# Kernel optimization log

Measured on AMD Instinct MI355X. Metric: run time of the kernel, lower is better.

The kernel has to match this reference:

```python
import jax, jax.numpy as jnp
import numpy as np

N = 50000   # nodes
E = 800000  # edges
B = 64      # graphs in batch
IN = 128    # in_features
HID = 64    # hidden_channels
H = 4       # head_count
C = 10      # out_classes
NEG = 0.2   # leaky relu negative slope
EPS = 1e-5  # batchnorm eps (eval mode, running mean 0 / var 1)


def _gat(x, edge_index, W, a_src, a_dst, b):
    """PyG GATConv (add_self_loops=False, concat=True), eval mode (no dropout)."""
    Hh, F = a_src.shape
    xW = (x @ W).reshape(-1, Hh, F)                       # [N,H,F]
    src, dst = edge_index[0], edge_index[1]
    e = (jnp.einsum('nhf,hf->nh', xW, a_src)[src]
         + jnp.einsum('nhf,hf->nh', xW, a_dst)[dst])      # [E,H]
    e = jnp.where(e > 0, e, NEG * e)                      # leaky relu
    m = jax.ops.segment_max(e, dst, num_segments=N)       # per-dst max
    m = jnp.where(jnp.isfinite(m), m, 0.0)
    p = jnp.exp(e - m[dst])
    denom = jax.ops.segment_sum(p, dst, num_segments=N)
    alpha = p / jnp.maximum(denom[dst], 1e-16)            # edge softmax over dst
    out = jax.ops.segment_sum(alpha[:, :, None] * xW[src], dst, num_segments=N)
    return out.reshape(-1, Hh * F) + b


def _bn_relu(y, g, be):
    # BatchNorm1d in eval mode with running_mean=0, running_var=1, then ReLU
    return jax.nn.relu(g * y / jnp.sqrt(1.0 + EPS) + be)


def setup_inputs():
    key = jax.random.key(0)
    ks = jax.random.split(key, 24)
    s = lambda k, shape: (jax.random.normal(k, shape, jnp.float32) * 0.05)
    z = lambda shape: jnp.zeros(shape, jnp.float32)
    o = lambda shape: jnp.ones(shape, jnp.float32)
    return {
        'acc_flag': 0,
        'x': jax.random.normal(ks[0], (N, IN), jnp.float32),
        'edge_index': jax.random.randint(ks[1], (2, E), 0, N),
        'batch': jnp.sort(jax.random.randint(ks[2], (N,), 0, B)),
        # layer 1: GATConv(IN -> HID, heads=H, concat)
        'W1': s(ks[3], (IN, H * HID)), 'a_src1': s(ks[4], (H, HID)), 'a_dst1': s(ks[5], (H, HID)), 'b1': z((H * HID,)),
        # proj: GATConv(H*HID -> HID, heads=1) + BN
        'W2': s(ks[6], (H * HID, HID)), 'a_src2': s(ks[7], (1, HID)), 'a_dst2': s(ks[8], (1, HID)), 'b2': z((HID,)), 'g2': o((HID,)), 'be2': z((HID,)),
        # block 1
        'W3': s(ks[9], (HID, HID)), 'a_src3': s(ks[10], (1, HID)), 'a_dst3': s(ks[11], (1, HID)), 'b3': z((HID,)), 'g3': o((HID,)), 'be3': z((HID,)),
        # block 2
        'W4': s(ks[12], (HID, HID)), 'a_src4': s(ks[13], (1, HID)), 'a_dst4': s(ks[14], (1, HID)), 'b4': z((HID,)), 'g4': o((HID,)), 'be4': z((HID,)),
        # MLP head
        'Wh1': s(ks[15], (HID, 128)), 'bh1': z((128,)),
        'Wh2': s(ks[16], (128, C)), 'bh2': z((C,)),
    }


def reference(acc_flag, x, edge_index, batch,
              W1, a_src1, a_dst1, b1,
              W2, a_src2, a_dst2, b2, g2, be2,
              W3, a_src3, a_dst3, b3, g3, be3,
              W4, a_src4, a_dst4, b4, g4, be4,
              Wh1, bh1, Wh2, bh2):
    # hardware GAT layer + ReLU (relu applied twice in original -> idempotent)
    x1 = jax.nn.relu(_gat(x, edge_index, W1, a_src1, a_dst1, b1))   # [N, H*HID]
    # projection block: residual base is zeros (shape mismatch H*HID vs HID)
    h = _bn_relu(_gat(x1, edge_index, W2, a_src2, a_dst2, b2), g2, be2)
    # residual blocks (shapes match -> x + relu(bn(y)))
    h = h + _bn_relu(_gat(h, edge_index, W3, a_src3, a_dst3, b3), g3, be3)
    h = h + _bn_relu(_gat(h, edge_index, W4, a_src4, a_dst4, b4), g4, be4)
    # global mean pool over graphs
    pooled = jax.ops.segment_sum(h, batch, num_segments=B)
    cnt = jnp.maximum(jax.ops.segment_sum(jnp.ones((N,), h.dtype), batch, num_segments=B), 1.0)
    hp = pooled / cnt[:, None]                                      # [B, HID]
    # MLP head
    return jax.nn.relu(hp @ Wh1 + bh1) @ Wh2 + bh2                  # [B, C]
```

## Files before the change

### kernel.cpp

```cpp
#include <hip/hip_runtime.h>

#define N_NODES 50000
#define N_EDGES 800000
#define N_GRAPHS 64
#define NEG_SLOPE 0.2f
#define BN_RSQ 0.9999950000374997f
#define NB_SCAN ((N_NODES + 255) / 256)

typedef __bf16 bf16x8 __attribute__((ext_vector_type(8)));
typedef float floatx4 __attribute__((ext_vector_type(4)));

__device__ __forceinline__ float lrelu(float v) { return v > 0.0f ? v : NEG_SLOPE * v; }

__device__ __forceinline__ float b2f(unsigned short u) {
    return __uint_as_float(((unsigned int)u) << 16);
}
__device__ __forceinline__ unsigned short f2b(float f) {
    unsigned int u = __float_as_uint(f);
    return (unsigned short)((u + 0x7fffu + ((u >> 16) & 1u)) >> 16);
}
__device__ __forceinline__ float blo(unsigned int d) { return __uint_as_float(d << 16); }
__device__ __forceinline__ float bhi(unsigned int d) { return __uint_as_float(d & 0xffff0000u); }

__global__ void k_deg(const int* __restrict__ ei, int* __restrict__ deg) {
    int e = blockIdx.x * blockDim.x + threadIdx.x;
    if (e < N_EDGES) atomicAdd(&deg[ei[N_EDGES + e]], 1);
}

__global__ __launch_bounds__(256) void k_offs(const int* __restrict__ deg, int* __restrict__ offs,
                                              int* __restrict__ total, const int* __restrict__ batch,
                                              int* __restrict__ bounds, int* __restrict__ bh) {
    __shared__ int lh[64];
    if (threadIdx.x < 64) lh[threadIdx.x] = 0;
    __syncthreads();
    if (blockIdx.x == 0 && threadIdx.x <= N_GRAPHS) {
        int g = threadIdx.x;
        int lo = 0, hi = N_NODES;
        while (lo < hi) {
            int mid = (lo + hi) >> 1;
            if (batch[mid] < g) lo = mid + 1; else hi = mid;
        }
        bounds[g] = lo;
    }
    int i = blockIdx.x * blockDim.x + threadIdx.x;
    int lane = threadIdx.x & 63;
    int v = (i < N_NODES) ? deg[i] : 0;
    int incl = v;
    for (int o = 1; o < 64; o <<= 1) {
        int t = __shfl_up(incl, o);
        if (lane >= o) incl += t;
    }
    int wtot = __shfl(incl, 63);
    int base = 0;
    if (lane == 0) base = atomicAdd(total, wtot);
    base = __shfl(base, 0);
    if (i < N_NODES) {
        offs[i] = base + incl - v;
        atomicAdd(&lh[min(v, 63)], 1);
    }
    __syncthreads();
    if (threadIdx.x < 64) bh[blockIdx.x * 64 + threadIdx.x] = lh[threadIdx.x];
}

__global__ __launch_bounds__(256) void k_pscan(const int* __restrict__ bh, int* __restrict__ bb) {
    __shared__ int partial[4][64];
    __shared__ int bbase[64];
    const int tid = threadIdx.x;
    const int b = tid & 63, q = tid >> 6;
    const int per = (NB_SCAN + 3) / 4;
    const int k0 = q * per, k1 = min(k0 + per, NB_SCAN);
    int s = 0;
    for (int k = k0; k < k1; ++k) s += bh[k * 64 + b];
    partial[q][b] = s;
    __syncthreads();
    if (tid < 64) {
        int tot = partial[0][tid] + partial[1][tid] + partial[2][tid] + partial[3][tid];
        int incl = tot;
        for (int o = 1; o < 64; o <<= 1) {
            int t2 = __shfl_up(incl, o);
            if (tid >= o) incl += t2;
        }
        bbase[tid] = incl - tot;
    }
    __syncthreads();
    int run = bbase[b];
    for (int q2 = 0; q2 < q; ++q2) run += partial[q2][b];
    for (int k = k0; k < k1; ++k) {
        bb[k * 64 + b] = run;
        run += bh[k * 64 + b];
    }
}

__global__ __launch_bounds__(256) void k_perm(const int* __restrict__ deg,
                                              const int* __restrict__ bb,
                                              int* __restrict__ perm) {
    __shared__ int lcnt[64];
    if (threadIdx.x < 64) lcnt[threadIdx.x] = 0;
    __syncthreads();
    int i = blockIdx.x * 256 + threadIdx.x;
    if (i < N_NODES) {
        int b = min(deg[i], 63);
        int r = atomicAdd(&lcnt[b], 1);
        perm[bb[blockIdx.x * 64 + b] + r] = i;
    }
}

__global__ void k_fill(const int* __restrict__ ei, const int* __restrict__ offs,
                       int* __restrict__ cur, int* __restrict__ csr_src) {
    int e = blockIdx.x * blockDim.x + threadIdx.x;
    if (e < N_EDGES) {
        int d = ei[N_EDGES + e];
        int pos = offs[d] + atomicAdd(&cur[d], 1);
        csr_src[pos] = ei[e];
    }
}

__global__ void k_prepw(const float* __restrict__ W1, const float* __restrict__ W2,
                        const float* __restrict__ W3, const float* __restrict__ W4,
                        unsigned short* __restrict__ Wt1, unsigned short* __restrict__ Wt2,
                        unsigned short* __restrict__ Wt3, unsigned short* __restrict__ Wt4) {
    int i = blockIdx.x * blockDim.x + threadIdx.x;
    if (i < 32768) {
        int k = i >> 8, n = i & 255;
        Wt1[n * 128 + k] = f2b(W1[i]);
    } else if (i < 49152) {
        int j = i - 32768;
        int k = j >> 6, n = j & 63;
        Wt2[n * 256 + k] = f2b(W2[j]);
    } else if (i < 53248) {
        int j = i - 49152;
        int k = j >> 6, n = j & 63;
        Wt3[n * 64 + k] = f2b(W3[j]);
    } else if (i < 57344) {
        int j = i - 53248;
        int k = j >> 6, n = j & 63;
        Wt4[n * 64 + k] = f2b(W4[j]);
    }
}

template <int K, int N, int HEADS, bool AF32>
__global__ __launch_bounds__(256) void k_mgemm(const void* __restrict__ Ap,
                                               const unsigned short* __restrict__ Bt,
                                               const float* __restrict__ asrc,
                                               const float* __restrict__ adst,
                                               unsigned short* __restrict__ out,
                                               float* __restrict__ es,
                                               float* __restrict__ ed, int rows) {
    constexpr int LDP = K + 8;
    __shared__ unsigned short As[64 * LDP];
    const int tid = threadIdx.x;
    const int r0 = blockIdx.x * 64;
    if (AF32) {
        const float* A = (const float*)Ap;
        for (int i = tid; i < 16 * K; i += 256) {
            int r = i / (K / 4), c4 = i % (K / 4);
            int row = r0 + r;
            float4 v = (row < rows) ? *(const float4*)&A[(size_t)row * K + c4 * 4]
                                    : make_float4(0.f, 0.f, 0.f, 0.f);
            ushort4 u;
            u.x = f2b(v.x); u.y = f2b(v.y); u.z = f2b(v.z); u.w = f2b(v.w);
            *(ushort4*)&As[r * LDP + c4 * 4] = u;
        }
    } else {
        const unsigned short* A = (const unsigned short*)Ap;
        for (int i = tid; i < 8 * K; i += 256) {
            int r = i / (K / 8), c8 = i % (K / 8);
            int row = r0 + r;
            uint4 v;
            if (row < rows) v = *(const uint4*)&A[(size_t)row * K + c8 * 8];
            else { v.x = v.y = v.z = v.w = 0; }
            *(uint4*)&As[r * LDP + c8 * 8] = v;
        }
    }
    __syncthreads();
    const int w = tid >> 6, lane = tid & 63;
    const int quad = lane >> 4, l16 = lane & 15;
    const int gr0 = r0 + w * 16 + quad * 4;
    bf16x8 afrag[K / 32];
#pragma unroll
    for (int kk = 0; kk < K / 32; ++kk)
        afrag[kk] = *(const bf16x8*)&As[(w * 16 + l16) * LDP + kk * 32 + quad * 8];
    float sacc[4] = {0.f, 0.f, 0.f, 0.f};
    float dacc[4] = {0.f, 0.f, 0.f, 0.f};
#pragma unroll 1
    for (int ct = 0; ct < N / 16; ++ct) {
        floatx4 acc = {0.f, 0.f, 0.f, 0.f};
#pragma unroll
        for (int kk = 0; kk < K / 32; ++kk) {
            const bf16x8 bfrag =
                *(const bf16x8*)&Bt[(size_t)(ct * 16 + l16) * K + kk * 32 + quad * 8];
            acc = __builtin_amdgcn_mfma_f32_16x16x32_bf16(afrag[kk], bfrag, acc, 0, 0, 0);
        }
        const int gc = ct * 16 + l16;
        const int hh = gc >> 6;
        const int f = gc & 63;
        const float as = asrc[hh * 64 + f];
        const float ad = adst[hh * 64 + f];
#pragma unroll
        for (int rg = 0; rg < 4; ++rg) {
            sacc[rg] = fmaf(acc[rg], as, sacc[rg]);
            dacc[rg] = fmaf(acc[rg], ad, dacc[rg]);
        }
#pragma unroll
        for (int rg = 0; rg < 4; ++rg) {
            int gr = gr0 + rg;
            if (gr < rows) out[(size_t)gr * N + gc] = f2b(acc[rg]);
        }
        if ((ct & 3) == 3) {
#pragma unroll
            for (int rg = 0; rg < 4; ++rg) {
                float s = sacc[rg], d = dacc[rg];
                for (int o = 1; o < 16; o <<= 1) {
                    s += __shfl_xor(s, o);
                    d += __shfl_xor(d, o);
                }
                if (l16 == 0) {
                    int gr = gr0 + rg;
                    if (gr < rows) {
                        es[(size_t)gr * HEADS + hh] = s;
                        ed[(size_t)gr * HEADS + hh] = d;
                    }
                }
                sacc[rg] = 0.f;
                dacc[rg] = 0.f;
            }
        }
    }
}

__global__ __launch_bounds__(256) void k_gat1(
    const unsigned short* __restrict__ xW, const float* __restrict__ es, const float* __restrict__ ed,
    const int* __restrict__ offs, const int* __restrict__ deg, const int* __restrict__ csr,
    const int* __restrict__ perm, const float* __restrict__ bias, unsigned short* __restrict__ out) {
    __shared__ float ps[4][4 * 68];
    __shared__ int sbuf[4][64];
    const int wv = threadIdx.x >> 6;
    const int lane = threadIdx.x & 63;
    const int grp = lane >> 4, t = lane & 15;
    const int h = t >> 2;
    const int pidx = blockIdx.x * 16 + wv * 4 + grp;
    if (pidx >= N_NODES) return;
    const int n = perm[pidx];
    const int off = offs[n];
    const int dg = deg[n];
    const float4 edv = *(const float4*)&ed[n * 4];

    float acc[16];
#pragma unroll
    for (int k = 0; k < 16; ++k) acc[k] = 0.f;
    float dsum = 0.f;

    for (int base = 0; base < dg; base += 16) {
        const int idx = base + t;
        int s_l = 0;
        float p0 = 0.f, p1 = 0.f, p2 = 0.f, p3 = 0.f;
        if (idx < dg) {
            s_l = csr[off + idx];
            const float4 ev = *(const float4*)&es[s_l * 4];
            p0 = __expf(lrelu(ev.x + edv.x));
            p1 = __expf(lrelu(ev.y + edv.y));
            p2 = __expf(lrelu(ev.z + edv.z));
            p3 = __expf(lrelu(ev.w + edv.w));
        }
        *(float4*)&ps[wv][grp * 68 + t * 4] = make_float4(p0, p1, p2, p3);
        sbuf[wv][grp * 16 + t] = s_l;
        const int cnt = min(16, dg - base);
        const int cntR = (cnt + 1) & ~1;
        for (int j = 0; j < cntR; j += 2) {
            const float pa = ps[wv][grp * 68 + j * 4 + h];
            const float pb = ps[wv][grp * 68 + (j + 1) * 4 + h];
            const int sa = sbuf[wv][grp * 16 + j];
            const int sb = sbuf[wv][grp * 16 + j + 1];
            const uint4 a0 = *(const uint4*)&xW[(size_t)sa * 256 + t * 16];
            const uint4 a1 = *(const uint4*)&xW[(size_t)sa * 256 + t * 16 + 8];
            const uint4 b0 = *(const uint4*)&xW[(size_t)sb * 256 + t * 16];
            const uint4 b1 = *(const uint4*)&xW[(size_t)sb * 256 + t * 16 + 8];
            dsum += pa + pb;
            acc[0]  = fmaf(pa, blo(a0.x), acc[0]);
            acc[1]  = fmaf(pa, bhi(a0.x), acc[1]);
            acc[2]  = fmaf(pa, blo(a0.y), acc[2]);
            acc[3]  = fmaf(pa, bhi(a0.y), acc[3]);
            acc[4]  = fmaf(pa, blo(a0.z), acc[4]);
            acc[5]  = fmaf(pa, bhi(a0.z), acc[5]);
            acc[6]  = fmaf(pa, blo(a0.w), acc[6]);
            acc[7]  = fmaf(pa, bhi(a0.w), acc[7]);
            acc[8]  = fmaf(pa, blo(a1.x), acc[8]);
            acc[9]  = fmaf(pa, bhi(a1.x), acc[9]);
            acc[10] = fmaf(pa, blo(a1.y), acc[10]);
            acc[11] = fmaf(pa, bhi(a1.y), acc[11]);
            acc[12] = fmaf(pa, blo(a1.z), acc[12]);
            acc[13] = fmaf(pa, bhi(a1.z), acc[13]);
            acc[14] = fmaf(pa, blo(a1.w), acc[14]);
            acc[15] = fmaf(pa, bhi(a1.w), acc[15]);
            acc[0]  = fmaf(pb, blo(b0.x), acc[0]);
            acc[1]  = fmaf(pb, bhi(b0.x), acc[1]);
            acc[2]  = fmaf(pb, blo(b0.y), acc[2]);
            acc[3]  = fmaf(pb, bhi(b0.y), acc[3]);
            acc[4]  = fmaf(pb, blo(b0.z), acc[4]);
            acc[5]  = fmaf(pb, bhi(b0.z), acc[5]);
            acc[6]  = fmaf(pb, blo(b0.w), acc[6]);
            acc[7]  = fmaf(pb, bhi(b0.w), acc[7]);
            acc[8]  = fmaf(pb, blo(b1.x), acc[8]);
            acc[9]  = fmaf(pb, bhi(b1.x), acc[9]);
            acc[10] = fmaf(pb, blo(b1.y), acc[10]);
            acc[11] = fmaf(pb, bhi(b1.y), acc[11]);
            acc[12] = fmaf(pb, blo(b1.z), acc[12]);
            acc[13] = fmaf(pb, bhi(b1.z), acc[13]);
            acc[14] = fmaf(pb, blo(b1.w), acc[14]);
            acc[15] = fmaf(pb, bhi(b1.w), acc[15]);
        }
    }
    const float inv = 1.0f / fmaxf(dsum, 1e-16f);
#pragma unroll
    for (int k4 = 0; k4 < 16; k4 += 4) {
        const int c = t * 16 + k4;
        const float4 bv = *(const float4*)&bias[c];
        ushort4 o4;
        o4.x = f2b(fmaxf(fmaf(acc[k4 + 0], inv, bv.x), 0.f));
        o4.y = f2b(fmaxf(fmaf(acc[k4 + 1], inv, bv.y), 0.f));
        o4.z = f2b(fmaxf(fmaf(acc[k4 + 2], inv, bv.z), 0.f));
        o4.w = f2b(fmaxf(fmaf(acc[k4 + 3], inv, bv.w), 0.f));
        *(ushort4*)&out[(size_t)n * 256 + c] = o4;
    }
}

template <bool RES>
__global__ __launch_bounds__(256) void k_gatL(
    const unsigned short* __restrict__ xW, const float* __restrict__ es, const float* __restrict__ ed,
    const int* __restrict__ offs, const int* __restrict__ deg, const int* __restrict__ csr,
    const int* __restrict__ perm, const float* __restrict__ bias, const float* __restrict__ gam,
    const float* __restrict__ bet, float* __restrict__ h, unsigned short* __restrict__ hb) {
    __shared__ float ps[4][64];
    __shared__ int sbuf[4][64];
    const int wv = threadIdx.x >> 6;
    const int lane = threadIdx.x & 63;
    const int grp = lane >> 3, t = lane & 7;
    const int pidx = blockIdx.x * 32 + wv * 8 + grp;
    if (pidx >= N_NODES) return;
    const int n = perm[pidx];
    const int off = offs[n];
    const int dg = deg[n];
    const float edn = ed[n];

    float acc[8];
#pragma unroll
    for (int k = 0; k < 8; ++k) acc[k] = 0.f;
    float dsum = 0.f;

    for (int base = 0; base < dg; base += 8) {
        const int idx = base + t;
        int s_l = 0;
        float p_l = 0.f;
        if (idx < dg) {
            s_l = csr[off + idx];
            p_l = __expf(lrelu(es[s_l] + edn));
        }
        ps[wv][grp * 8 + t] = p_l;
        sbuf[wv][grp * 8 + t] = s_l;
        const int cnt = min(8, dg - base);
        const int cntR = (cnt + 1) & ~1;
        for (int j = 0; j < cntR; j += 2) {
            const float pa = ps[wv][grp * 8 + j];
            const float pb = ps[wv][grp * 8 + j + 1];
            const int sa = sbuf[wv][grp * 8 + j];
            const int sb = sbuf[wv][grp * 8 + j + 1];
            const uint4 a = *(const uint4*)&xW[(size_t)sa * 64 + t * 8];
            const uint4 b = *(const uint4*)&xW[(size_t)sb * 64 + t * 8];
            dsum += pa + pb;
            acc[0] = fmaf(pa, blo(a.x), acc[0]);
            acc[1] = fmaf(pa, bhi(a.x), acc[1]);
            acc[2] = fmaf(pa, blo(a.y), acc[2]);
            acc[3] = fmaf(pa, bhi(a.y), acc[3]);
            acc[4] = fmaf(pa, blo(a.z), acc[4]);
            acc[5] = fmaf(pa, bhi(a.z), acc[5]);
            acc[6] = fmaf(pa, blo(a.w), acc[6]);
            acc[7] = fmaf(pa, bhi(a.w), acc[7]);
            acc[0] = fmaf(pb, blo(b.x), acc[0]);
            acc[1] = fmaf(pb, bhi(b.x), acc[1]);
            acc[2] = fmaf(pb, blo(b.y), acc[2]);
            acc[3] = fmaf(pb, bhi(b.y), acc[3]);
            acc[4] = fmaf(pb, blo(b.z), acc[4]);
            acc[5] = fmaf(pb, bhi(b.z), acc[5]);
            acc[6] = fmaf(pb, blo(b.w), acc[6]);
            acc[7] = fmaf(pb, bhi(b.w), acc[7]);
        }
    }
    const float inv = 1.0f / fmaxf(dsum, 1e-16f);
    const int c0 = t * 8;
    float hn[8];
#pragma unroll
    for (int k = 0; k < 8; ++k) {
        const int c = c0 + k;
        const float y = fmaf(acc[k], inv, bias[c]);
        const float z = fmaxf(fmaf(gam[c] * y, BN_RSQ, bet[c]), 0.f);
        hn[k] = RES ? h[(size_t)n * 64 + c] + z : z;
    }
    *(float4*)&h[(size_t)n * 64 + c0] = make_float4(hn[0], hn[1], hn[2], hn[3]);
    *(float4*)&h[(size_t)n * 64 + c0 + 4] = make_float4(hn[4], hn[5], hn[6], hn[7]);
    ushort4 u0, u1;
    u0.x = f2b(hn[0]); u0.y = f2b(hn[1]); u0.z = f2b(hn[2]); u0.w = f2b(hn[3]);
    u1.x = f2b(hn[4]); u1.y = f2b(hn[5]); u1.z = f2b(hn[6]); u1.w = f2b(hn[7]);
    *(ushort4*)&hb[(size_t)n * 64 + c0] = u0;
    *(ushort4*)&hb[(size_t)n * 64 + c0 + 4] = u1;
}

__global__ __launch_bounds__(256) void k_pool2(const float* __restrict__ h,
                                               const int* __restrict__ bounds,
                                               float* __restrict__ hp) {
    __shared__ float part[4][64];
    const int g = blockIdx.x;
    const int lane = threadIdx.x & 63;
    const int wid = threadIdx.x >> 6;
    const int s = bounds[g], e = bounds[g + 1];
    float acc = 0.f;
    for (int n = s + wid; n < e; n += 4) acc += h[n * 64 + lane];
    part[wid][lane] = acc;
    __syncthreads();
    if (wid == 0) {
        float v = part[0][lane] + part[1][lane] + part[2][lane] + part[3][lane];
        hp[g * 64 + lane] = v / fmaxf((float)(e - s), 1.0f);
    }
}

__global__ __launch_bounds__(256) void k_head(const float* __restrict__ hpg,
                                              const float* __restrict__ Wh1,
                                              const float* __restrict__ bh1,
                                              const float* __restrict__ Wh2,
                                              const float* __restrict__ bh2,
                                              float* __restrict__ out) {
    __shared__ float hp[64 * 64];
    __shared__ float t1[64 * 128];
    const int tid = threadIdx.x;
    for (int i = tid; i < 64 * 64; i += 256) hp[i] = hpg[i];
    __syncthreads();
    for (int i = tid; i < 64 * 128; i += 256) {
        int g = i >> 7, j = i & 127;
        float s = bh1[j];
        for (int k = 0; k < 64; ++k) s = fmaf(hp[g * 64 + k], Wh1[k * 128 + j], s);
        t1[i] = fmaxf(s, 0.f);
    }
    __syncthreads();
    for (int i = tid; i < 640; i += 256) {
        int g = i / 10, j = i - g * 10;
        float s = bh2[j];
        for (int k = 0; k < 128; ++k) s = fmaf(t1[g * 128 + k], Wh2[k * 10 + j], s);
        out[i] = s;
    }
}

extern "C" void kernel_launch(void* const* d_in, const int* in_sizes, int n_in,
                              void* d_out, int out_size, void* d_ws, size_t ws_size,
                              hipStream_t stream) {
    const float* x = (const float*)d_in[1];
    const int* ei = (const int*)d_in[2];
    const int* batch = (const int*)d_in[3];
    const float* W1 = (const float*)d_in[4];
    const float* a_src1 = (const float*)d_in[5];
    const float* a_dst1 = (const float*)d_in[6];
    const float* b1 = (const float*)d_in[7];
    const float* W2 = (const float*)d_in[8];
    const float* a_src2 = (const float*)d_in[9];
    const float* a_dst2 = (const float*)d_in[10];
    const float* b2 = (const float*)d_in[11];
    const float* g2 = (const float*)d_in[12];
    const float* be2 = (const float*)d_in[13];
    const float* W3 = (const float*)d_in[14];
    const float* a_src3 = (const float*)d_in[15];
    const float* a_dst3 = (const float*)d_in[16];
    const float* b3 = (const float*)d_in[17];
    const float* g3 = (const float*)d_in[18];
    const float* be3 = (const float*)d_in[19];
    const float* W4 = (const float*)d_in[20];
    const float* a_src4 = (const float*)d_in[21];
    const float* a_dst4 = (const float*)d_in[22];
    const float* b4 = (const float*)d_in[23];
    const float* g4 = (const float*)d_in[24];
    const float* be4 = (const float*)d_in[25];
    const float* Wh1 = (const float*)d_in[26];
    const float* bh1 = (const float*)d_in[27];
    const float* Wh2 = (const float*)d_in[28];
    const float* bh2 = (const float*)d_in[29];
    float* out = (float*)d_out;

    char* p = (char*)d_ws;
    auto alloc = [&](size_t bytes) {
        void* r = (void*)p;
        p += (bytes + 255) & ~(size_t)255;
        return r;
    };
    unsigned short* bufA = (unsigned short*)alloc((size_t)N_NODES * 256 * 2);
    unsigned short* x1b = (unsigned short*)alloc((size_t)N_NODES * 256 * 2);
    float* h = (float*)alloc((size_t)N_NODES * 64 * 4);
    unsigned short* hb = (unsigned short*)alloc((size_t)N_NODES * 64 * 2);
    float* es1 = (float*)alloc((size_t)N_NODES * 4 * 4);
    float* ed1 = (float*)alloc((size_t)N_NODES * 4 * 4);
    float* esL = (float*)alloc((size_t)N_NODES * 4);
    float* edL = (float*)alloc((size_t)N_NODES * 4);
    int* offs = (int*)alloc((size_t)N_NODES * 4);
    int* csr = (int*)alloc((size_t)N_EDGES * 4);
    int* perm = (int*)alloc((size_t)N_NODES * 4);
    int* bounds = (int*)alloc((size_t)(N_GRAPHS + 1) * 4);
    int* bh_hist = (int*)alloc((size_t)NB_SCAN * 64 * 4);
    int* bb = (int*)alloc((size_t)NB_SCAN * 64 * 4);
    float* hpool = (float*)alloc((size_t)N_GRAPHS * 64 * 4);
    unsigned short* Wt1 = (unsigned short*)alloc((size_t)128 * 256 * 2);
    unsigned short* Wt2 = (unsigned short*)alloc((size_t)256 * 64 * 2);
    unsigned short* Wt3 = (unsigned short*)alloc((size_t)64 * 64 * 2);
    unsigned short* Wt4 = (unsigned short*)alloc((size_t)64 * 64 * 2);
    char* z0 = p;
    int* deg = (int*)alloc((size_t)N_NODES * 4);
    int* cur = (int*)alloc((size_t)N_NODES * 4);
    int* total = (int*)alloc(256);
    size_t zbytes = (size_t)(p - z0);
    hipMemsetAsync(z0, 0, zbytes, stream);

    const int edgeBlocks = (N_EDGES + 255) / 256;
    const int mgemmBlocks = (N_NODES + 63) / 64;
    const int gat1Blocks = (N_NODES + 15) / 16;
    const int gatLBlocks = (N_NODES + 31) / 32;

    k_prepw<<<(57344 + 255) / 256, 256, 0, stream>>>(W1, W2, W3, W4, Wt1, Wt2, Wt3, Wt4);

    k_deg<<<edgeBlocks, 256, 0, stream>>>(ei, deg);
    k_offs<<<NB_SCAN, 256, 0, stream>>>(deg, offs, total, batch, bounds, bh_hist);
    k_pscan<<<1, 256, 0, stream>>>(bh_hist, bb);
    k_perm<<<NB_SCAN, 256, 0, stream>>>(deg, bb, perm);
    k_fill<<<edgeBlocks, 256, 0, stream>>>(ei, offs, cur, csr);

    k_mgemm<128, 256, 4, true><<<mgemmBlocks, 256, 0, stream>>>(x, Wt1, a_src1, a_dst1,
                                                                bufA, es1, ed1, N_NODES);
    k_gat1<<<gat1Blocks, 256, 0, stream>>>(bufA, es1, ed1, offs, deg, csr, perm, b1, x1b);

    k_mgemm<256, 64, 1, false><<<mgemmBlocks, 256, 0, stream>>>(x1b, Wt2, a_src2, a_dst2,
                                                                bufA, esL, edL, N_NODES);
    k_gatL<false><<<gatLBlocks, 256, 0, stream>>>(bufA, esL, edL, offs, deg, csr, perm, b2, g2, be2, h, hb);

    k_mgemm<64, 64, 1, false><<<mgemmBlocks, 256, 0, stream>>>(hb, Wt3, a_src3, a_dst3,
                                                               bufA, esL, edL, N_NODES);
    k_gatL<true><<<gatLBlocks, 256, 0, stream>>>(bufA, esL, edL, offs, deg, csr, perm, b3, g3, be3, h, hb);

    k_mgemm<64, 64, 1, false><<<mgemmBlocks, 256, 0, stream>>>(hb, Wt4, a_src4, a_dst4,
                                                               bufA, esL, edL, N_NODES);
    k_gatL<true><<<gatLBlocks, 256, 0, stream>>>(bufA, esL, edL, offs, deg, csr, perm, b4, g4, be4, h, hb);

    k_pool2<<<N_GRAPHS, 256, 0, stream>>>(h, bounds, hpool);
    k_head<<<1, 256, 0, stream>>>(hpool, Wh1, bh1, Wh2, bh2, out);
}
```

Before: 530.4 us.

## Fuse next-layer projection GEMM into GAT aggregation epilogues and merge prep kernels

Each GAT aggregation kernel now multiplies its freshly computed node row by the next layer's weight matrix in its epilogue. It writes xW and the attention source/destination scores directly, which removes three separate MFMA GEMM launches and the round trip of the 256-wide x1 and hb intermediates through global memory. The epilogue GEMMs use scalar FMAs with per-lane weight loads rather than matrix cores, which adds ALU work and weight traffic inside latency-bound gather kernels. Weight conversion and the degree count are merged into one launch, and the degree-bucket permutation order is reversed so high-degree nodes come first.

```diff
diff --git a/kernel.cpp b/kernel.cpp
--- a/kernel.cpp
+++ b/kernel.cpp
@@ -22,9 +22,23 @@
 __device__ __forceinline__ float blo(unsigned int d) { return __uint_as_float(d << 16); }
 __device__ __forceinline__ float bhi(unsigned int d) { return __uint_as_float(d & 0xffff0000u); }
 
-__global__ void k_deg(const int* __restrict__ ei, int* __restrict__ deg) {
-    int e = blockIdx.x * blockDim.x + threadIdx.x;
-    if (e < N_EDGES) atomicAdd(&deg[ei[N_EDGES + e]], 1);
+__global__ void k_prep(const int* __restrict__ ei, int* __restrict__ deg,
+                       const float* __restrict__ W1, const float* __restrict__ W2,
+                       const float* __restrict__ W3, const float* __restrict__ W4,
+                       unsigned short* __restrict__ Wt1, unsigned short* __restrict__ W2b,
+                       unsigned short* __restrict__ W3b, unsigned short* __restrict__ W4b) {
+    int i = blockIdx.x * 256 + threadIdx.x;
+    if (i < 32768) {
+        int k = i >> 8, n = i & 255;
+        Wt1[n * 128 + k] = f2b(W1[i]);
+    } else if (i < 49152) {
+        W2b[i - 32768] = f2b(W2[i - 32768]);
+    } else if (i < 53248) {
+        W3b[i - 49152] = f2b(W3[i - 49152]);
+    } else if (i < 57344) {
+        W4b[i - 53248] = f2b(W4[i - 53248]);
+    }
+    if (i < N_EDGES) atomicAdd(&deg[ei[N_EDGES + i]], 1);
 }
 
 __global__ __launch_bounds__(256) void k_offs(const int* __restrict__ deg, int* __restrict__ offs,
@@ -56,7 +70,7 @@
     base = __shfl(base, 0);
     if (i < N_NODES) {
         offs[i] = base + incl - v;
-        atomicAdd(&lh[min(v, 63)], 1);
+        atomicAdd(&lh[63 - min(v, 63)], 1);
     }
     __syncthreads();
     if (threadIdx.x < 64) bh[blockIdx.x * 64 + threadIdx.x] = lh[threadIdx.x];
@@ -99,7 +113,7 @@
     __syncthreads();
     int i = blockIdx.x * 256 + threadIdx.x;
     if (i < N_NODES) {
-        int b = min(deg[i], 63);
+        int b = 63 - min(deg[i], 63);
         int r = atomicAdd(&lcnt[b], 1);
         perm[bb[blockIdx.x * 64 + b] + r] = i;
     }
@@ -112,29 +126,6 @@
         int d = ei[N_EDGES + e];
         int pos = offs[d] + atomicAdd(&cur[d], 1);
         csr_src[pos] = ei[e];
-    }
-}
-
-__global__ void k_prepw(const float* __restrict__ W1, const float* __restrict__ W2,
-                        const float* __restrict__ W3, const float* __restrict__ W4,
-                        unsigned short* __restrict__ Wt1, unsigned short* __restrict__ Wt2,
-                        unsigned short* __restrict__ Wt3, unsigned short* __restrict__ Wt4) {
-    int i = blockIdx.x * blockDim.x + threadIdx.x;
-    if (i < 32768) {
-        int k = i >> 8, n = i & 255;
-        Wt1[n * 128 + k] = f2b(W1[i]);
-    } else if (i < 49152) {
-        int j = i - 32768;
-        int k = j >> 6, n = j & 63;
-        Wt2[n * 256 + k] = f2b(W2[j]);
-    } else if (i < 53248) {
-        int j = i - 49152;
-        int k = j >> 6, n = j & 63;
-        Wt3[n * 64 + k] = f2b(W3[j]);
-    } else if (i < 57344) {
-        int j = i - 53248;
-        int k = j >> 6, n = j & 63;
-        Wt4[n * 64 + k] = f2b(W4[j]);
     }
 }
 
@@ -231,19 +222,23 @@
 __global__ __launch_bounds__(256) void k_gat1(
     const unsigned short* __restrict__ xW, const float* __restrict__ es, const float* __restrict__ ed,
     const int* __restrict__ offs, const int* __restrict__ deg, const int* __restrict__ csr,
-    const int* __restrict__ perm, const float* __restrict__ bias, unsigned short* __restrict__ out) {
+    const int* __restrict__ perm, const float* __restrict__ bias,
+    const unsigned short* __restrict__ W2b, const float* __restrict__ asrc2,
+    const float* __restrict__ adst2, unsigned short* __restrict__ xW2,
+    float* __restrict__ es2, float* __restrict__ ed2) {
     __shared__ float ps[4][4 * 68];
     __shared__ int sbuf[4][64];
+    __shared__ unsigned short x1buf[4][1024];
     const int wv = threadIdx.x >> 6;
     const int lane = threadIdx.x & 63;
     const int grp = lane >> 4, t = lane & 15;
     const int h = t >> 2;
     const int pidx = blockIdx.x * 16 + wv * 4 + grp;
-    if (pidx >= N_NODES) return;
     const int n = perm[pidx];
     const int off = offs[n];
     const int dg = deg[n];
     const float4 edv = *(const float4*)&ed[n * 4];
+    const int cb = t * 16;
 
     float acc[16];
 #pragma unroll
@@ -267,14 +262,14 @@
         const int cnt = min(16, dg - base);
         const int cntR = (cnt + 1) & ~1;
         for (int j = 0; j < cntR; j += 2) {
-            const float pa = ps[wv][grp * 68 + j * 4 + h];
+            const float pa = ps[wv][grp * 68 + (j + 0) * 4 + h];
             const float pb = ps[wv][grp * 68 + (j + 1) * 4 + h];
-            const int sa = sbuf[wv][grp * 16 + j];
+            const int sa = sbuf[wv][grp * 16 + j + 0];
             const int sb = sbuf[wv][grp * 16 + j + 1];
-            const uint4 a0 = *(const uint4*)&xW[(size_t)sa * 256 + t * 16];
-            const uint4 a1 = *(const uint4*)&xW[(size_t)sa * 256 + t * 16 + 8];
-            const uint4 b0 = *(const uint4*)&xW[(size_t)sb * 256 + t * 16];
-            const uint4 b1 = *(const uint4*)&xW[(size_t)sb * 256 + t * 16 + 8];
+            const uint4 a0 = *(const uint4*)&xW[(size_t)sa * 256 + cb];
+            const uint4 a1 = *(const uint4*)&xW[(size_t)sa * 256 + cb + 8];
+            const uint4 b0 = *(const uint4*)&xW[(size_t)sb * 256 + cb];
+            const uint4 b1 = *(const uint4*)&xW[(size_t)sb * 256 + cb + 8];
             dsum += pa + pb;
             acc[0]  = fmaf(pa, blo(a0.x), acc[0]);
             acc[1]  = fmaf(pa, bhi(a0.x), acc[1]);
@@ -311,27 +306,60 @@
         }
     }
     const float inv = 1.0f / fmaxf(dsum, 1e-16f);
+    unsigned short* x1s = &x1buf[wv][grp * 256];
 #pragma unroll
     for (int k4 = 0; k4 < 16; k4 += 4) {
-        const int c = t * 16 + k4;
+        const int c = cb + k4;
         const float4 bv = *(const float4*)&bias[c];
         ushort4 o4;
         o4.x = f2b(fmaxf(fmaf(acc[k4 + 0], inv, bv.x), 0.f));
         o4.y = f2b(fmaxf(fmaf(acc[k4 + 1], inv, bv.y), 0.f));
         o4.z = f2b(fmaxf(fmaf(acc[k4 + 2], inv, bv.z), 0.f));
         o4.w = f2b(fmaxf(fmaf(acc[k4 + 3], inv, bv.w), 0.f));
-        *(ushort4*)&out[(size_t)n * 256 + c] = o4;
-    }
-}
-
-template <bool RES>
+        *(ushort4*)&x1s[c] = o4;
+    }
+    const int c0 = t * 4;
+    float og0 = 0.f, og1 = 0.f, og2 = 0.f, og3 = 0.f;
+    for (int k = 0; k < 256; k += 2) {
+        const unsigned int xp = *(const unsigned int*)&x1s[k];
+        const float xk0 = blo(xp), xk1 = bhi(xp);
+        const ushort4 w0 = *(const ushort4*)&W2b[k * 64 + c0];
+        const ushort4 w1 = *(const ushort4*)&W2b[(k + 1) * 64 + c0];
+        og0 = fmaf(xk0, b2f(w0.x), og0);
+        og1 = fmaf(xk0, b2f(w0.y), og1);
+        og2 = fmaf(xk0, b2f(w0.z), og2);
+        og3 = fmaf(xk0, b2f(w0.w), og3);
+        og0 = fmaf(xk1, b2f(w1.x), og0);
+        og1 = fmaf(xk1, b2f(w1.y), og1);
+        og2 = fmaf(xk1, b2f(w1.z), og2);
+        og3 = fmaf(xk1, b2f(w1.w), og3);
+    }
+    const float4 a2s = *(const float4*)&asrc2[c0];
+    const float4 a2d = *(const float4*)&adst2[c0];
+    float s2 = og0 * a2s.x + og1 * a2s.y + og2 * a2s.z + og3 * a2s.w;
+    float d2 = og0 * a2d.x + og1 * a2d.y + og2 * a2d.z + og3 * a2d.w;
+    for (int o = 1; o < 16; o <<= 1) {
+        s2 += __shfl_xor(s2, o);
+        d2 += __shfl_xor(d2, o);
+    }
+    if (t == 0) { es2[n] = s2; ed2[n] = d2; }
+    ushort4 xw;
+    xw.x = f2b(og0); xw.y = f2b(og1); xw.z = f2b(og2); xw.w = f2b(og3);
+    *(ushort4*)&xW2[(size_t)n * 64 + c0] = xw;
+}
+
+template <bool RES, bool NEXT>
 __global__ __launch_bounds__(256) void k_gatL(
     const unsigned short* __restrict__ xW, const float* __restrict__ es, const float* __restrict__ ed,
     const int* __restrict__ offs, const int* __restrict__ deg, const int* __restrict__ csr,
     const int* __restrict__ perm, const float* __restrict__ bias, const float* __restrict__ gam,
-    const float* __restrict__ bet, float* __restrict__ h, unsigned short* __restrict__ hb) {
+    const float* __restrict__ bet, float* __restrict__ h,
+    const unsigned short* __restrict__ Wn, const float* __restrict__ asn,
+    const float* __restrict__ adn, unsigned short* __restrict__ xwn,
+    float* __restrict__ esn, float* __restrict__ edn) {
     __shared__ float ps[4][64];
     __shared__ int sbuf[4][64];
+    __shared__ unsigned short hbuf[4][512];
     const int wv = threadIdx.x >> 6;
     const int lane = threadIdx.x & 63;
     const int grp = lane >> 3, t = lane & 7;
@@ -340,7 +368,8 @@
     const int n = perm[pidx];
     const int off = offs[n];
     const int dg = deg[n];
-    const float edn = ed[n];
+    const float edv = ed[n];
+    const int cb = t * 8;
 
     float acc[8];
 #pragma unroll
@@ -353,7 +382,7 @@
         float p_l = 0.f;
         if (idx < dg) {
             s_l = csr[off + idx];
-            p_l = __expf(lrelu(es[s_l] + edn));
+            p_l = __expf(lrelu(es[s_l] + edv));
         }
         ps[wv][grp * 8 + t] = p_l;
         sbuf[wv][grp * 8 + t] = s_l;
@@ -364,8 +393,8 @@
             const float pb = ps[wv][grp * 8 + j + 1];
             const int sa = sbuf[wv][grp * 8 + j];
             const int sb = sbuf[wv][grp * 8 + j + 1];
-            const uint4 a = *(const uint4*)&xW[(size_t)sa * 64 + t * 8];
-            const uint4 b = *(const uint4*)&xW[(size_t)sb * 64 + t * 8];
+            const uint4 a = *(const uint4*)&xW[(size_t)sa * 64 + cb];
+            const uint4 b = *(const uint4*)&xW[(size_t)sb * 64 + cb];
             dsum += pa + pb;
             acc[0] = fmaf(pa, blo(a.x), acc[0]);
             acc[1] = fmaf(pa, bhi(a.x), acc[1]);
@@ -386,22 +415,67 @@
         }
     }
     const float inv = 1.0f / fmaxf(dsum, 1e-16f);
-    const int c0 = t * 8;
     float hn[8];
 #pragma unroll
     for (int k = 0; k < 8; ++k) {
-        const int c = c0 + k;
+        const int c = cb + k;
         const float y = fmaf(acc[k], inv, bias[c]);
         const float z = fmaxf(fmaf(gam[c] * y, BN_RSQ, bet[c]), 0.f);
         hn[k] = RES ? h[(size_t)n * 64 + c] + z : z;
     }
-    *(float4*)&h[(size_t)n * 64 + c0] = make_float4(hn[0], hn[1], hn[2], hn[3]);
-    *(float4*)&h[(size_t)n * 64 + c0 + 4] = make_float4(hn[4], hn[5], hn[6], hn[7]);
-    ushort4 u0, u1;
-    u0.x = f2b(hn[0]); u0.y = f2b(hn[1]); u0.z = f2b(hn[2]); u0.w = f2b(hn[3]);
-    u1.x = f2b(hn[4]); u1.y = f2b(hn[5]); u1.z = f2b(hn[6]); u1.w = f2b(hn[7]);
-    *(ushort4*)&hb[(size_t)n * 64 + c0] = u0;
-    *(ushort4*)&hb[(size_t)n * 64 + c0 + 4] = u1;
+    *(float4*)&h[(size_t)n * 64 + cb] = make_float4(hn[0], hn[1], hn[2], hn[3]);
+    *(float4*)&h[(size_t)n * 64 + cb + 4] = make_float4(hn[4], hn[5], hn[6], hn[7]);
+    if (NEXT) {
+        unsigned short* hbl = &hbuf[wv][grp * 64];
+        ushort4 u0, u1;
+        u0.x = f2b(hn[0]); u0.y = f2b(hn[1]); u0.z = f2b(hn[2]); u0.w = f2b(hn[3]);
+        u1.x = f2b(hn[4]); u1.y = f2b(hn[5]); u1.z = f2b(hn[6]); u1.w = f2b(hn[7]);
+        *(ushort4*)&hbl[cb] = u0;
+        *(ushort4*)&hbl[cb + 4] = u1;
+        float og[8];
+#pragma unroll
+        for (int k = 0; k < 8; ++k) og[k] = 0.f;
+        for (int k = 0; k < 64; k += 2) {
+            const unsigned int xp = *(const unsigned int*)&hbl[k];
+            const float xk0 = blo(xp), xk1 = bhi(xp);
+            const uint4 w0 = *(const uint4*)&Wn[k * 64 + cb];
+            const uint4 w1 = *(const uint4*)&Wn[(k + 1) * 64 + cb];
+            og[0] = fmaf(xk0, blo(w0.x), og[0]);
+            og[1] = fmaf(xk0, bhi(w0.x), og[1]);
+            og[2] = fmaf(xk0, blo(w0.y), og[2]);
+            og[3] = fmaf(xk0, bhi(w0.y), og[3]);
+            og[4] = fmaf(xk0, blo(w0.z), og[4]);
+            og[5] = fmaf(xk0, bhi(w0.z), og[5]);
+            og[6] = fmaf(xk0, blo(w0.w), og[6]);
+            og[7] = fmaf(xk0, bhi(w0.w), og[7]);
+            og[0] = fmaf(xk1, blo(w1.x), og[0]);
+            og[1] = fmaf(xk1, bhi(w1.x), og[1]);
+            og[2] = fmaf(xk1, blo(w1.y), og[2]);
+            og[3] = fmaf(xk1, bhi(w1.y), og[3]);
+            og[4] = fmaf(xk1, blo(w1.z), og[4]);
+            og[5] = fmaf(xk1, bhi(w1.z), og[5]);
+            og[6] = fmaf(xk1, blo(w1.w), og[6]);
+            og[7] = fmaf(xk1, bhi(w1.w), og[7]);
+        }
+        float s = 0.f, d = 0.f;
+#pragma unroll
+        for (int kk = 0; kk < 8; kk += 4) {
+            const float4 asv = *(const float4*)&asn[cb + kk];
+            const float4 adv = *(const float4*)&adn[cb + kk];
+            s += og[kk] * asv.x + og[kk + 1] * asv.y + og[kk + 2] * asv.z + og[kk + 3] * asv.w;
+            d += og[kk] * adv.x + og[kk + 1] * adv.y + og[kk + 2] * adv.z + og[kk + 3] * adv.w;
+        }
+        for (int o = 1; o < 8; o <<= 1) {
+            s += __shfl_xor(s, o);
+            d += __shfl_xor(d, o);
+        }
+        if (t == 0) { esn[n] = s; edn[n] = d; }
+        ushort4 x0, x1v;
+        x0.x = f2b(og[0]); x0.y = f2b(og[1]); x0.z = f2b(og[2]); x0.w = f2b(og[3]);
+        x1v.x = f2b(og[4]); x1v.y = f2b(og[5]); x1v.z = f2b(og[6]); x1v.w = f2b(og[7]);
+        *(ushort4*)&xwn[(size_t)n * 64 + cb] = x0;
+        *(ushort4*)&xwn[(size_t)n * 64 + cb + 4] = x1v;
+    }
 }
 
 __global__ __launch_bounds__(256) void k_pool2(const float* __restrict__ h,
@@ -489,13 +563,14 @@
         return r;
     };
     unsigned short* bufA = (unsigned short*)alloc((size_t)N_NODES * 256 * 2);
-    unsigned short* x1b = (unsigned short*)alloc((size_t)N_NODES * 256 * 2);
+    unsigned short* bufB = (unsigned short*)alloc((size_t)N_NODES * 64 * 2);
     float* h = (float*)alloc((size_t)N_NODES * 64 * 4);
-    unsigned short* hb = (unsigned short*)alloc((size_t)N_NODES * 64 * 2);
     float* es1 = (float*)alloc((size_t)N_NODES * 4 * 4);
     float* ed1 = (float*)alloc((size_t)N_NODES * 4 * 4);
-    float* esL = (float*)alloc((size_t)N_NODES * 4);
-    float* edL = (float*)alloc((size_t)N_NODES * 4);
+    float* esA = (float*)alloc((size_t)N_NODES * 4);
+    float* edA = (float*)alloc((size_t)N_NODES * 4);
+    float* esB = (float*)alloc((size_t)N_NODES * 4);
+    float* edB = (float*)alloc((size_t)N_NODES * 4);
     int* offs = (int*)alloc((size_t)N_NODES * 4);
     int* csr = (int*)alloc((size_t)N_EDGES * 4);
     int* perm = (int*)alloc((size_t)N_NODES * 4);
@@ -504,9 +579,9 @@
     int* bb = (int*)alloc((size_t)NB_SCAN * 64 * 4);
     float* hpool = (float*)alloc((size_t)N_GRAPHS * 64 * 4);
     unsigned short* Wt1 = (unsigned short*)alloc((size_t)128 * 256 * 2);
-    unsigned short* Wt2 = (unsigned short*)alloc((size_t)256 * 64 * 2);
-    unsigned short* Wt3 = (unsigned short*)alloc((size_t)64 * 64 * 2);
-    unsigned short* Wt4 = (unsigned short*)alloc((size_t)64 * 64 * 2);
+    unsigned short* W2b = (unsigned short*)alloc((size_t)256 * 64 * 2);
+    unsigned short* W3b = (unsigned short*)alloc((size_t)64 * 64 * 2);
+    unsigned short* W4b = (unsigned short*)alloc((size_t)64 * 64 * 2);
     char* z0 = p;
     int* deg = (int*)alloc((size_t)N_NODES * 4);
     int* cur = (int*)alloc((size_t)N_NODES * 4);
@@ -519,9 +594,8 @@
     const int gat1Blocks = (N_NODES + 15) / 16;
     const int gatLBlocks = (N_NODES + 31) / 32;
 
-    k_prepw<<<(57344 + 255) / 256, 256, 0, stream>>>(W1, W2, W3, W4, Wt1, Wt2, Wt3, Wt4);
-
-    k_deg<<<edgeBlocks, 256, 0, stream>>>(ei, deg);
+    k_prep<<<edgeBlocks, 256, 0, stream>>>(ei, deg, W1, W2, W3, W4, Wt1, W2b, W3b, W4b);
+
     k_offs<<<NB_SCAN, 256, 0, stream>>>(deg, offs, total, batch, bounds, bh_hist);
     k_pscan<<<1, 256, 0, stream>>>(bh_hist, bb);
     k_perm<<<NB_SCAN, 256, 0, stream>>>(deg, bb, perm);
@@ -529,19 +603,19 @@
 
     k_mgemm<128, 256, 4, true><<<mgemmBlocks, 256, 0, stream>>>(x, Wt1, a_src1, a_dst1,
                                                                 bufA, es1, ed1, N_NODES);
-    k_gat1<<<gat1Blocks, 256, 0, stream>>>(bufA, es1, ed1, offs, deg, csr, perm, b1, x1b);
-
-    k_mgemm<256, 64, 1, false><<<mgemmBlocks, 256, 0, stream>>>(x1b, Wt2, a_src2, a_dst2,
-                                                                bufA, esL, edL, N_NODES);
-    k_gatL<false><<<gatLBlocks, 256, 0, stream>>>(bufA, esL, edL, offs, deg, csr, perm, b2, g2, be2, h, hb);
-
-    k_mgemm<64, 64, 1, false><<<mgemmBlocks, 256, 0, stream>>>(hb, Wt3, a_src3, a_dst3,
-                                                               bufA, esL, edL, N_NODES);
-    k_gatL<true><<<gatLBlocks, 256, 0, stream>>>(bufA, esL, edL, offs, deg, csr, perm, b3, g3, be3, h, hb);
-
-    k_mgemm<64, 64, 1, false><<<mgemmBlocks, 256, 0, stream>>>(hb, Wt4, a_src4, a_dst4,
-                                                               bufA, esL, edL, N_NODES);
-    k_gatL<true><<<gatLBlocks, 256, 0, stream>>>(bufA, esL, edL, offs, deg, csr, perm, b4, g4, be4, h, hb);
+    k_gat1<<<gat1Blocks, 256, 0, stream>>>(bufA, es1, ed1, offs, deg, csr, perm, b1,
+                                           W2b, a_src2, a_dst2, bufB, esA, edA);
+    k_gatL<false, true><<<gatLBlocks, 256, 0, stream>>>(bufB, esA, edA, offs, deg, csr, perm,
+                                                        b2, g2, be2, h, W3b, a_src3, a_dst3,
+                                                        bufA, esB, edB);
+    k_gatL<true, true><<<gatLBlocks, 256, 0, stream>>>(bufA, esB, edB, offs, deg, csr, perm,
+                                                       b3, g3, be3, h, W4b, a_src4, a_dst4,
+                                                       bufB, esA, edA);
+    k_gatL<true, false><<<gatLBlocks, 256, 0, stream>>>(bufB, esA, edA, offs, deg, csr, perm,
+                                                        b4, g4, be4, h, (const unsigned short*)nullptr,
+                                                        (const float*)nullptr, (const float*)nullptr,
+                                                        (unsigned short*)nullptr,
+                                                        (float*)nullptr, (float*)nullptr);
 
     k_pool2<<<N_GRAPHS, 256, 0, stream>>>(h, bounds, hpool);
     k_head<<<1, 256, 0, stream>>>(hpool, Wh1, bh1, Wh2, bh2, out);
```

Result: slower. 577.2 us (+8.8%).
